# Kernel optimization log

Measured on AMD Instinct MI355X. Metric: run time of the kernel, lower is better.

The kernel has to match this reference:

```python
import jax, jax.numpy as jnp
import numpy as np

H_IMG, W_IMG = 32, 32   # img_dim
HID = 256               # hidden_size
B = 128                 # batch


def setup_inputs() -> dict:
    key = jax.random.key(0)
    k1, k2, k3, k4 = jax.random.split(key, 4)
    x = jax.random.normal(k1, (B, H_IMG * W_IMG), dtype=jnp.float32)
    w_ih = jax.random.normal(k2, (4 * HID, 1), dtype=jnp.float32) * 0.1
    w_hh = jax.random.normal(k3, (4 * HID, HID), dtype=jnp.float32) * 0.05
    bias = jax.random.normal(k4, (4 * HID,), dtype=jnp.float32) * 0.1
    return {"x": x, "w_ih": w_ih, "w_hh": w_hh, "bias": bias}


def _mdlstm(x, w_ih, w_hh, bias):
    # x: [B, H*W] in row-major pixel order (pixel_idx = row*W + col)
    Bb = x.shape[0]
    xg = x.reshape(Bb, H_IMG, W_IMG).transpose(1, 2, 0)  # [H, W, B]
    wih_vec = w_ih[:, 0]  # input_size == 1 -> linear is scalar * row-vector

    def cell(x_pix, h_up, s_up, h_left, s_left):
        # Same weight_hh is applied to both directional hidden states; for
        # boundary pixels the corresponding h/s are zeros, so the gating in
        # the original code (skip when row==0 / col==0) holds identically.
        gates = (x_pix[:, None] * wih_vec[None, :]
                 + (h_up + h_left) @ w_hh.T
                 + bias)                                  # [B, 4*HID]
        i, f, g, o = jnp.split(gates, 4, axis=1)
        i = jax.nn.sigmoid(i)
        f = jax.nn.sigmoid(f)
        g = jnp.tanh(g)
        o = jax.nn.sigmoid(o)
        s = f * (s_up + s_left) + i * g                   # shared forgetgate for both dims
        h = o * jnp.tanh(s)
        return h, s

    zeros = jnp.zeros((Bb, HID), x.dtype)

    def row_step(carry, x_row):
        h_up_row, s_up_row = carry                        # [W, B, HID] each

        def col_step(c, inp):
            h_left, s_left = c
            x_pix, h_up, s_up = inp
            h, s = cell(x_pix, h_up, s_up, h_left, s_left)
            return (h, s), (h, s)

        _, (h_row, s_row) = jax.lax.scan(col_step, (zeros, zeros),
                                         (x_row, h_up_row, s_up_row))
        return (h_row, s_row), h_row

    init = (jnp.zeros((W_IMG, Bb, HID), x.dtype),
            jnp.zeros((W_IMG, Bb, HID), x.dtype))
    _, h_all = jax.lax.scan(row_step, init, xg)           # [H, W, B, HID]
    # torch.cat(h_matrix, 1): pixels ordered row-major, each [B, HID]
    return h_all.transpose(2, 0, 1, 3).reshape(Bb, H_IMG * W_IMG * HID)


def reference(x, w_ih, w_hh, bias):
    return _mdlstm(x, w_ih, w_hh, bias)
```

## Files before the change

### kernel.cpp

```cpp
#include <hip/hip_runtime.h>
#include <math.h>


#define HIMG 32
#define WIMG 32
#define BATCH 128
#define HID 256
#define BH (BATCH * HID)
#define SLAB (32 * 128 * 256)

#define WSTRIDE 136

typedef double f64x4 __attribute__((ext_vector_type(4)));

__global__ __launch_bounds__(256, 4)
void mdlstm_diag_kernel(const float* __restrict__ x,
                        const float* __restrict__ wih,
                        const float* __restrict__ whh,
                        const float* __restrict__ bias,
                        float* __restrict__ out,
                        double* __restrict__ hbuf,
                        double* __restrict__ sbuf,
                        int d, int rlo)
{
    __shared__ double lds[4096];
    double* A_lds = lds;
    float*  W_lds = (float*)(lds + 1024);
    double* G_lds = lds;

    const int tid = threadIdx.x;
    const int id  = blockIdx.x;
    const int cellIdx = id >> 5;
    const int tileIdx = id & 31;
    const int ktile = tileIdx & 7;
    const int b4    = tileIdx >> 3;
    const int k0 = ktile * 32;
    const int b0 = b4 * 32;

    const int r = rlo + cellIdx;
    const int c = d - r;
    const int rc = r * WIMG + c;

    const int prev = (d & 1) ^ 1;
    const int cur  = d & 1;
    const double* hp = hbuf + (size_t)prev * SLAB;
    const double* sp = sbuf + (size_t)prev * SLAB;
    double* hc = hbuf + (size_t)cur * SLAB;
    double* sc = sbuf + (size_t)cur * SLAB;

    const bool has_up   = (r > 0);
    const bool has_left = (c > 0);
    const double* hu = hp + (size_t)(r - 1) * BH;
    const double* hl = hp + (size_t)r * BH;

    const int lane = tid & 63;
    const int wid  = tid >> 6;
    const int wb0  = (wid & 1) * 16;
    const int wf0  = (wid >> 1) * 64;
    const int cc   = lane & 15;
    const int gg   = lane >> 4;

    int layout;
    {
        double pa = (cc == 1) ? 1.0 : 0.0;
        double pb = (cc == 2) ? 1.0 : 0.0;
        f64x4 pc = {0.0, 0.0, 0.0, 0.0};
        pc = __builtin_amdgcn_mfma_f64_16x16x4f64(pa, pb, pc, 0, 0, 0);
        double s = fabs(pc[0]) + fabs(pc[1]) + fabs(pc[2]) + fabs(pc[3]);
        #pragma unroll
        for (int off = 32; off > 0; off >>= 1) s += __shfl_xor(s, off, 64);
        unsigned long long h0 = __ballot(lane == 2  && pc[1] == 4.0);
        unsigned long long h1 = __ballot(lane == 18 && pc[0] == 4.0);
        unsigned long long h2 = __ballot(lane == 1  && pc[2] == 4.0);
        unsigned long long h3 = __ballot(lane == 33 && pc[0] == 4.0);
        layout = -1;
        if (s == 4.0) {
            if (h0) layout = 0;
            else if (h1) layout = 1;
            else if (h2) layout = 2;
            else if (h3) layout = 3;
        }
    }
    const bool use_mfma = (layout >= 0);

    const int a_row = tid >> 4;
    const int a_kp  = tid & 15;
    const size_t ga0 = (size_t)(b0 + a_row) * HID + 2 * a_kp;
    const size_t ga1 = ga0 + (size_t)16 * HID;
    const float* w_src[4];
    int w_phi[4], w_kq[4];
    #pragma unroll
    for (int p = 0; p < 4; p++) {
        int u = tid + p * 256;
        int phi = u >> 3, kq = u & 7;
        int F = (phi >> 5) * 256 + k0 + (phi & 31);
        w_src[p] = whh + (size_t)F * HID + 4 * kq;
        w_phi[p] = phi; w_kq[p] = kq;
    }

    f64x4 acc[4];
    #pragma unroll
    for (int ft = 0; ft < 4; ft++) acc[ft] = (f64x4){0.0, 0.0, 0.0, 0.0};

    double2 pu0, pu1, pl0, pl1;
    float4 pw[4];
    {
        const double2 z = {0.0, 0.0};
        pu0 = has_up   ? *(const double2*)(hu + ga0) : z;
        pu1 = has_up   ? *(const double2*)(hu + ga1) : z;
        pl0 = has_left ? *(const double2*)(hl + ga0) : z;
        pl1 = has_left ? *(const double2*)(hl + ga1) : z;
        #pragma unroll
        for (int p = 0; p < 4; p++)
            pw[p] = *(const float4*)(w_src[p]);
    }

    for (int ck = 0; ck < 8; ck++) {
        __syncthreads();
        {
            const int k = 2 * a_kp;
            const double s0x = pu0.x + pl0.x, s0y = pu0.y + pl0.y;
            const double s1x = pu1.x + pl1.x, s1y = pu1.y + pl1.y;
            A_lds[ k      * 32 + ((a_row      + k    ) & 31)] = s0x;
            A_lds[(k + 1) * 32 + ((a_row      + k + 1) & 31)] = s0y;
            A_lds[ k      * 32 + ((a_row + 16 + k    ) & 31)] = s1x;
            A_lds[(k + 1) * 32 + ((a_row + 16 + k + 1) & 31)] = s1y;
        }
        #pragma unroll
        for (int p = 0; p < 4; p++) {
            const int kb = 4 * w_kq[p];
            W_lds[(kb + 0) * WSTRIDE + w_phi[p]] = pw[p].x;
            W_lds[(kb + 1) * WSTRIDE + w_phi[p]] = pw[p].y;
            W_lds[(kb + 2) * WSTRIDE + w_phi[p]] = pw[p].z;
            W_lds[(kb + 3) * WSTRIDE + w_phi[p]] = pw[p].w;
        }
        __syncthreads();

        if (ck < 7) {
            const int kg = (ck + 1) * 32;
            const double2 z = {0.0, 0.0};
            pu0 = has_up   ? *(const double2*)(hu + ga0 + kg) : z;
            pu1 = has_up   ? *(const double2*)(hu + ga1 + kg) : z;
            pl0 = has_left ? *(const double2*)(hl + ga0 + kg) : z;
            pl1 = has_left ? *(const double2*)(hl + ga1 + kg) : z;
            #pragma unroll
            for (int p = 0; p < 4; p++)
                pw[p] = *(const float4*)(w_src[p] + kg);
        }

        if (use_mfma) {
            #pragma unroll
            for (int t = 0; t < 8; t++) {
                const int kq = t * 4 + gg;
                const double aval = A_lds[kq * 32 + ((wb0 + cc + kq) & 31)];
                const float* wrow = &W_lds[kq * WSTRIDE + wf0 + cc];
                #pragma unroll
                for (int ft = 0; ft < 4; ft++) {
                    const double bval = (double)wrow[ft * 16];
                    acc[ft] = __builtin_amdgcn_mfma_f64_16x16x4f64(aval, bval, acc[ft], 0, 0, 0);
                }
            }
        } else {
            for (int k = 0; k < 32; k++) {
                double av[4], wv4[4];
                #pragma unroll
                for (int b = 0; b < 4; b++)
                    av[b] = A_lds[k * 32 + ((wb0 + 4 * gg + b + k) & 31)];
                #pragma unroll
                for (int ft = 0; ft < 4; ft++)
                    wv4[ft] = (double)W_lds[k * WSTRIDE + wf0 + ft * 16 + cc];
                #pragma unroll
                for (int ft = 0; ft < 4; ft++)
                    #pragma unroll
                    for (int b = 0; b < 4; b++)
                        acc[ft][b] = fma(av[b], wv4[ft], acc[ft][b]);
            }
        }
    }

    __syncthreads();
    const int slay = use_mfma ? layout : 0;
    #pragma unroll
    for (int ft = 0; ft < 4; ft++) {
        #pragma unroll
        for (int b = 0; b < 4; b++) {
            const int rA = (slay & 1) ? (gg + 4 * b) : (4 * gg + b);
            const int m  = (slay >= 2) ? cc : rA;
            const int n  = (slay >= 2) ? rA : cc;
            const int phi  = wf0 + ft * 16 + n;
            const int brow = wb0 + m;
            G_lds[phi * 32 + ((brow + phi) & 31)] = acc[ft][b];
        }
    }
    __syncthreads();

    const int ec = tid & 31;
    const int eb = tid >> 5;
    const int k = k0 + ec;
    double wv[4], bv[4];
    #pragma unroll
    for (int g = 0; g < 4; g++) {
        wv[g] = (double)wih[g * 256 + k];
        bv[g] = (double)bias[g * 256 + k];
    }
    #pragma unroll
    for (int i = 0; i < 4; i++) {
        const int bl = eb + 8 * i;
        const int b = b0 + bl;
        double gate[4];
        #pragma unroll
        for (int g = 0; g < 4; g++) {
            const int phi = g * 32 + ec;
            gate[g] = G_lds[phi * 32 + ((bl + phi) & 31)];
        }
        const double xp = (double)x[b * (HIMG * WIMG) + rc];
        const double su = has_up   ? sp[(size_t)(r - 1) * BH + b * HID + k] : 0.0;
        const double sl = has_left ? sp[(size_t)r * BH + b * HID + k]       : 0.0;
        const double gi = gate[0] + xp * wv[0] + bv[0];
        const double gf = gate[1] + xp * wv[1] + bv[1];
        const double gg2 = gate[2] + xp * wv[2] + bv[2];
        const double go = gate[3] + xp * wv[3] + bv[3];
        const double iv = 1.0 / (1.0 + exp(-gi));
        const double fv = 1.0 / (1.0 + exp(-gf));
        const double gv = tanh(gg2);
        const double ov = 1.0 / (1.0 + exp(-go));
        const double sv = fv * (su + sl) + iv * gv;
        const double hv = ov * tanh(sv);
        sc[(size_t)r * BH + b * HID + k] = sv;
        hc[(size_t)r * BH + b * HID + k] = hv;
        out[(size_t)b * (HIMG * WIMG * HID) + (size_t)rc * HID + k] = (float)hv;
    }
}

extern "C" void kernel_launch(void* const* d_in, const int* in_sizes, int n_in,
                              void* d_out, int out_size, void* d_ws, size_t ws_size,
                              hipStream_t stream) {
    const float* x    = (const float*)d_in[0];
    const float* wih  = (const float*)d_in[1];
    const float* whh  = (const float*)d_in[2];
    const float* bias = (const float*)d_in[3];
    float* out = (float*)d_out;

    double* hbuf = (double*)d_ws;
    double* sbuf = hbuf + (size_t)2 * SLAB;

    for (int d = 0; d < HIMG + WIMG - 1; d++) {
        int rlo = d - (WIMG - 1); if (rlo < 0) rlo = 0;
        int rhi = d < (HIMG - 1) ? d : (HIMG - 1);
        int nc = rhi - rlo + 1;
        mdlstm_diag_kernel<<<dim3(nc * 32), 256, 0, stream>>>(
            x, wih, whh, bias, out, hbuf, sbuf, d, rlo);
    }
}
```

Baseline: 3.143 ms.

## Replace per-diagonal kernel launches with a persistent cooperative kernel using grid sync

Replaces the 63 separate per-anti-diagonal kernel launches with a single persistent cooperative kernel of 1024 blocks. It loops over diagonals internally and uses grid.sync between them. Per-block setup (MFMA layout probe, input-weight and bias loads) is hoisted out of the diagonal loop. This removes launch overhead and repeated setup, but every block must wait at each grid barrier even when idle on short diagonals. If cooperative launch is unavailable or occupancy is insufficient, it falls back to the old multi-launch path.

```diff
diff --git a/kernel.cpp b/kernel.cpp
--- a/kernel.cpp
+++ b/kernel.cpp
@@ -1,4 +1,5 @@
 #include <hip/hip_runtime.h>
+#include <hip/hip_cooperative_groups.h>
 #include <math.h>
 
 
@@ -13,15 +14,16 @@
 
 typedef double f64x4 __attribute__((ext_vector_type(4)));
 
+namespace cg = cooperative_groups;
+
 __global__ __launch_bounds__(256, 4)
-void mdlstm_diag_kernel(const float* __restrict__ x,
-                        const float* __restrict__ wih,
-                        const float* __restrict__ whh,
-                        const float* __restrict__ bias,
-                        float* __restrict__ out,
-                        double* __restrict__ hbuf,
-                        double* __restrict__ sbuf,
-                        int d, int rlo)
+void mdlstm_persistent(const float* __restrict__ x,
+                       const float* __restrict__ wih,
+                       const float* __restrict__ whh,
+                       const float* __restrict__ bias,
+                       float* __restrict__ out,
+                       double* __restrict__ hbuf,
+                       double* __restrict__ sbuf)
 {
     __shared__ double lds[4096];
     double* A_lds = lds;
@@ -29,29 +31,13 @@
     double* G_lds = lds;
 
     const int tid = threadIdx.x;
-    const int id  = blockIdx.x;
-    const int cellIdx = id >> 5;
-    const int tileIdx = id & 31;
+    const int bid = blockIdx.x;
+    const int cellSlot = bid >> 5;
+    const int tileIdx = bid & 31;
     const int ktile = tileIdx & 7;
     const int b4    = tileIdx >> 3;
     const int k0 = ktile * 32;
     const int b0 = b4 * 32;
-
-    const int r = rlo + cellIdx;
-    const int c = d - r;
-    const int rc = r * WIMG + c;
-
-    const int prev = (d & 1) ^ 1;
-    const int cur  = d & 1;
-    const double* hp = hbuf + (size_t)prev * SLAB;
-    const double* sp = sbuf + (size_t)prev * SLAB;
-    double* hc = hbuf + (size_t)cur * SLAB;
-    double* sc = sbuf + (size_t)cur * SLAB;
-
-    const bool has_up   = (r > 0);
-    const bool has_left = (c > 0);
-    const double* hu = hp + (size_t)(r - 1) * BH;
-    const double* hl = hp + (size_t)r * BH;
 
     const int lane = tid & 63;
     const int wid  = tid >> 6;
@@ -82,6 +68,261 @@
         }
     }
     const bool use_mfma = (layout >= 0);
+    const int slay = use_mfma ? layout : 0;
+
+    const int a_row = tid >> 4;
+    const int a_kp  = tid & 15;
+    const size_t ga0 = (size_t)(b0 + a_row) * HID + 2 * a_kp;
+    const size_t ga1 = ga0 + (size_t)16 * HID;
+    const float* w_src[4];
+    int w_phi[4], w_kq[4];
+    #pragma unroll
+    for (int p = 0; p < 4; p++) {
+        int u = tid + p * 256;
+        int phi = u >> 3, kq = u & 7;
+        int F = (phi >> 5) * 256 + k0 + (phi & 31);
+        w_src[p] = whh + (size_t)F * HID + 4 * kq;
+        w_phi[p] = phi; w_kq[p] = kq;
+    }
+
+    const int ec = tid & 31;
+    const int eb = tid >> 5;
+    const int kE = k0 + ec;
+    double wvE[4], bvE[4];
+    #pragma unroll
+    for (int g = 0; g < 4; g++) {
+        wvE[g] = (double)wih[g * 256 + kE];
+        bvE[g] = (double)bias[g * 256 + kE];
+    }
+
+    cg::grid_group grid = cg::this_grid();
+
+    for (int d = 0; d < HIMG + WIMG - 1; d++) {
+        int rlo = d - (WIMG - 1); if (rlo < 0) rlo = 0;
+        int rhi = d < (HIMG - 1) ? d : (HIMG - 1);
+        int nc = rhi - rlo + 1;
+
+        if (cellSlot < nc) {
+            const int r = rlo + cellSlot;
+            const int c = d - r;
+            const int rc = r * WIMG + c;
+
+            const int prev = (d & 1) ^ 1;
+            const int cur  = d & 1;
+            const double* hp = hbuf + (size_t)prev * SLAB;
+            const double* sp = sbuf + (size_t)prev * SLAB;
+            double* hc = hbuf + (size_t)cur * SLAB;
+            double* sc = sbuf + (size_t)cur * SLAB;
+
+            const bool has_up   = (r > 0);
+            const bool has_left = (c > 0);
+            const double* hu = hp + (size_t)(r - 1) * BH;
+            const double* hl = hp + (size_t)r * BH;
+
+            f64x4 acc[4];
+            #pragma unroll
+            for (int ft = 0; ft < 4; ft++) acc[ft] = (f64x4){0.0, 0.0, 0.0, 0.0};
+
+            double2 pu0, pu1, pl0, pl1;
+            float4 pw[4];
+            {
+                const double2 z = {0.0, 0.0};
+                pu0 = has_up   ? *(const double2*)(hu + ga0) : z;
+                pu1 = has_up   ? *(const double2*)(hu + ga1) : z;
+                pl0 = has_left ? *(const double2*)(hl + ga0) : z;
+                pl1 = has_left ? *(const double2*)(hl + ga1) : z;
+                #pragma unroll
+                for (int p = 0; p < 4; p++)
+                    pw[p] = *(const float4*)(w_src[p]);
+            }
+
+            for (int ck = 0; ck < 8; ck++) {
+                __syncthreads();
+                {
+                    const int k = 2 * a_kp;
+                    const double s0x = pu0.x + pl0.x, s0y = pu0.y + pl0.y;
+                    const double s1x = pu1.x + pl1.x, s1y = pu1.y + pl1.y;
+                    A_lds[ k      * 32 + ((a_row      + k    ) & 31)] = s0x;
+                    A_lds[(k + 1) * 32 + ((a_row      + k + 1) & 31)] = s0y;
+                    A_lds[ k      * 32 + ((a_row + 16 + k    ) & 31)] = s1x;
+                    A_lds[(k + 1) * 32 + ((a_row + 16 + k + 1) & 31)] = s1y;
+                }
+                #pragma unroll
+                for (int p = 0; p < 4; p++) {
+                    const int kb = 4 * w_kq[p];
+                    W_lds[(kb + 0) * WSTRIDE + w_phi[p]] = pw[p].x;
+                    W_lds[(kb + 1) * WSTRIDE + w_phi[p]] = pw[p].y;
+                    W_lds[(kb + 2) * WSTRIDE + w_phi[p]] = pw[p].z;
+                    W_lds[(kb + 3) * WSTRIDE + w_phi[p]] = pw[p].w;
+                }
+                __syncthreads();
+
+                if (ck < 7) {
+                    const int kg = (ck + 1) * 32;
+                    const double2 z = {0.0, 0.0};
+                    pu0 = has_up   ? *(const double2*)(hu + ga0 + kg) : z;
+                    pu1 = has_up   ? *(const double2*)(hu + ga1 + kg) : z;
+                    pl0 = has_left ? *(const double2*)(hl + ga0 + kg) : z;
+                    pl1 = has_left ? *(const double2*)(hl + ga1 + kg) : z;
+                    #pragma unroll
+                    for (int p = 0; p < 4; p++)
+                        pw[p] = *(const float4*)(w_src[p] + kg);
+                }
+
+                if (use_mfma) {
+                    #pragma unroll
+                    for (int t = 0; t < 8; t++) {
+                        const int kq = t * 4 + gg;
+                        const double aval = A_lds[kq * 32 + ((wb0 + cc + kq) & 31)];
+                        const float* wrow = &W_lds[kq * WSTRIDE + wf0 + cc];
+                        #pragma unroll
+                        for (int ft = 0; ft < 4; ft++) {
+                            const double bval = (double)wrow[ft * 16];
+                            acc[ft] = __builtin_amdgcn_mfma_f64_16x16x4f64(aval, bval, acc[ft], 0, 0, 0);
+                        }
+                    }
+                } else {
+                    for (int k = 0; k < 32; k++) {
+                        double av[4], wv4[4];
+                        #pragma unroll
+                        for (int b = 0; b < 4; b++)
+                            av[b] = A_lds[k * 32 + ((wb0 + 4 * gg + b + k) & 31)];
+                        #pragma unroll
+                        for (int ft = 0; ft < 4; ft++)
+                            wv4[ft] = (double)W_lds[k * WSTRIDE + wf0 + ft * 16 + cc];
+                        #pragma unroll
+                        for (int ft = 0; ft < 4; ft++)
+                            #pragma unroll
+                            for (int b = 0; b < 4; b++)
+                                acc[ft][b] = fma(av[b], wv4[ft], acc[ft][b]);
+                    }
+                }
+            }
+
+            double xp4[4], su4[4], sl4[4];
+            #pragma unroll
+            for (int i = 0; i < 4; i++) {
+                const int b = b0 + eb + 8 * i;
+                xp4[i] = (double)x[b * (HIMG * WIMG) + rc];
+                su4[i] = has_up   ? sp[(size_t)(r - 1) * BH + b * HID + kE] : 0.0;
+                sl4[i] = has_left ? sp[(size_t)r * BH + b * HID + kE]       : 0.0;
+            }
+
+            __syncthreads();
+            #pragma unroll
+            for (int ft = 0; ft < 4; ft++) {
+                #pragma unroll
+                for (int b = 0; b < 4; b++) {
+                    const int rA = (slay & 1) ? (gg + 4 * b) : (4 * gg + b);
+                    const int m  = (slay >= 2) ? cc : rA;
+                    const int n  = (slay >= 2) ? rA : cc;
+                    const int phi  = wf0 + ft * 16 + n;
+                    const int brow = wb0 + m;
+                    G_lds[phi * 32 + ((brow + phi) & 31)] = acc[ft][b];
+                }
+            }
+            __syncthreads();
+
+            #pragma unroll
+            for (int i = 0; i < 4; i++) {
+                const int bl = eb + 8 * i;
+                const int b = b0 + bl;
+                double gate[4];
+                #pragma unroll
+                for (int g = 0; g < 4; g++) {
+                    const int phi = g * 32 + ec;
+                    gate[g] = G_lds[phi * 32 + ((bl + phi) & 31)];
+                }
+                const double gi = gate[0] + xp4[i] * wvE[0] + bvE[0];
+                const double gf = gate[1] + xp4[i] * wvE[1] + bvE[1];
+                const double gG = gate[2] + xp4[i] * wvE[2] + bvE[2];
+                const double go = gate[3] + xp4[i] * wvE[3] + bvE[3];
+                const double iv = 1.0 / (1.0 + exp(-gi));
+                const double fv = 1.0 / (1.0 + exp(-gf));
+                const double gv = tanh(gG);
+                const double ov = 1.0 / (1.0 + exp(-go));
+                const double sv = fv * (su4[i] + sl4[i]) + iv * gv;
+                const double hv = ov * tanh(sv);
+                sc[(size_t)r * BH + b * HID + kE] = sv;
+                hc[(size_t)r * BH + b * HID + kE] = hv;
+                out[(size_t)b * (HIMG * WIMG * HID) + (size_t)rc * HID + kE] = (float)hv;
+            }
+        }
+
+        __threadfence();
+        grid.sync();
+    }
+}
+
+__global__ __launch_bounds__(256, 4)
+void mdlstm_diag_kernel(const float* __restrict__ x,
+                        const float* __restrict__ wih,
+                        const float* __restrict__ whh,
+                        const float* __restrict__ bias,
+                        float* __restrict__ out,
+                        double* __restrict__ hbuf,
+                        double* __restrict__ sbuf,
+                        int d, int rlo)
+{
+    __shared__ double lds[4096];
+    double* A_lds = lds;
+    float*  W_lds = (float*)(lds + 1024);
+    double* G_lds = lds;
+
+    const int tid = threadIdx.x;
+    const int id  = blockIdx.x;
+    const int cellIdx = id >> 5;
+    const int tileIdx = id & 31;
+    const int ktile = tileIdx & 7;
+    const int b4    = tileIdx >> 3;
+    const int k0 = ktile * 32;
+    const int b0 = b4 * 32;
+
+    const int r = rlo + cellIdx;
+    const int c = d - r;
+    const int rc = r * WIMG + c;
+
+    const int prev = (d & 1) ^ 1;
+    const int cur  = d & 1;
+    const double* hp = hbuf + (size_t)prev * SLAB;
+    const double* sp = sbuf + (size_t)prev * SLAB;
+    double* hc = hbuf + (size_t)cur * SLAB;
+    double* sc = sbuf + (size_t)cur * SLAB;
+
+    const bool has_up   = (r > 0);
+    const bool has_left = (c > 0);
+    const double* hu = hp + (size_t)(r - 1) * BH;
+    const double* hl = hp + (size_t)r * BH;
+
+    const int lane = tid & 63;
+    const int wid  = tid >> 6;
+    const int wb0  = (wid & 1) * 16;
+    const int wf0  = (wid >> 1) * 64;
+    const int cc   = lane & 15;
+    const int gg   = lane >> 4;
+
+    int layout;
+    {
+        double pa = (cc == 1) ? 1.0 : 0.0;
+        double pb = (cc == 2) ? 1.0 : 0.0;
+        f64x4 pc = {0.0, 0.0, 0.0, 0.0};
+        pc = __builtin_amdgcn_mfma_f64_16x16x4f64(pa, pb, pc, 0, 0, 0);
+        double s = fabs(pc[0]) + fabs(pc[1]) + fabs(pc[2]) + fabs(pc[3]);
+        #pragma unroll
+        for (int off = 32; off > 0; off >>= 1) s += __shfl_xor(s, off, 64);
+        unsigned long long h0 = __ballot(lane == 2  && pc[1] == 4.0);
+        unsigned long long h1 = __ballot(lane == 18 && pc[0] == 4.0);
+        unsigned long long h2 = __ballot(lane == 1  && pc[2] == 4.0);
+        unsigned long long h3 = __ballot(lane == 33 && pc[0] == 4.0);
+        layout = -1;
+        if (s == 4.0) {
+            if (h0) layout = 0;
+            else if (h1) layout = 1;
+            else if (h2) layout = 2;
+            else if (h3) layout = 3;
+        }
+    }
+    const bool use_mfma = (layout >= 0);
 
     const int a_row = tid >> 4;
     const int a_kp  = tid & 15;
@@ -244,6 +485,23 @@
     double* hbuf = (double*)d_ws;
     double* sbuf = hbuf + (size_t)2 * SLAB;
 
+    static int coop = -1;
+    if (coop < 0) {
+        int maxB = 0;
+        hipError_t e = hipOccupancyMaxActiveBlocksPerMultiprocessor(
+            &maxB, mdlstm_persistent, 256, 0);
+        coop = (e == hipSuccess && maxB >= 4) ? 1 : 0;
+    }
+
+    if (coop) {
+        void* args[] = {(void*)&x, (void*)&wih, (void*)&whh, (void*)&bias,
+                        (void*)&out, (void*)&hbuf, (void*)&sbuf};
+        hipError_t e = hipLaunchCooperativeKernel(
+            mdlstm_persistent, dim3(1024), dim3(256), args, 0, stream);
+        if (e == hipSuccess) return;
+        coop = 0;
+    }
+
     for (int d = 0; d < HIMG + WIMG - 1; d++) {
         int rlo = d - (WIMG - 1); if (rlo < 0) rlo = 0;
         int rhi = d < (HIMG - 1) ? d : (HIMG - 1);
```

Measured after the change: 3.112 ms. No clear change (-1.0%).

## Remap block indices for XCD locality, vectorize W LDS stores, prefetch epilogue loads

Applied to the files above, without the earlier changes.

Block indices are remapped so that the eight consecutive blocks (id & 7) land on different (cell, batch-tile) groups sharing the same k-tile, which aims to improve L2 reuse of the w_hh slices across the XCDs. The grid is padded to a multiple of 64, and surplus blocks return early. The W tile in LDS is transposed to a phi-major layout with stride 36, so each thread stores it with one float4 write instead of four scalar writes. The x and previous cell-state loads for the epilogue are issued before the G_lds write barrier so their latency overlaps the MFMA drain, at the cost of extra registers.

```diff
diff --git a/kernel.cpp b/kernel.cpp
--- a/kernel.cpp
+++ b/kernel.cpp
@@ -9,7 +9,7 @@
 #define BH (BATCH * HID)
 #define SLAB (32 * 128 * 256)
 
-#define WSTRIDE 136
+#define PSTR 36
 
 typedef double f64x4 __attribute__((ext_vector_type(4)));
 
@@ -21,7 +21,7 @@
                         float* __restrict__ out,
                         double* __restrict__ hbuf,
                         double* __restrict__ sbuf,
-                        int d, int rlo)
+                        int d, int rlo, int nc)
 {
     __shared__ double lds[4096];
     double* A_lds = lds;
@@ -30,10 +30,15 @@
 
     const int tid = threadIdx.x;
     const int id  = blockIdx.x;
-    const int cellIdx = id >> 5;
-    const int tileIdx = id & 31;
-    const int ktile = tileIdx & 7;
-    const int b4    = tileIdx >> 3;
+
+    const int rx    = id & 7;
+    const int q     = id >> 3;
+    const int ktile = q & 7;
+    const int ghi   = q >> 3;
+    const int g     = ghi * 8 + rx;
+    if (g >= nc * 4) return;
+    const int cellIdx = g >> 2;
+    const int b4      = g & 3;
     const int k0 = ktile * 32;
     const int b0 = b4 * 32;
 
@@ -88,14 +93,14 @@
     const size_t ga0 = (size_t)(b0 + a_row) * HID + 2 * a_kp;
     const size_t ga1 = ga0 + (size_t)16 * HID;
     const float* w_src[4];
-    int w_phi[4], w_kq[4];
+    int w_pos[4];
     #pragma unroll
     for (int p = 0; p < 4; p++) {
         int u = tid + p * 256;
         int phi = u >> 3, kq = u & 7;
         int F = (phi >> 5) * 256 + k0 + (phi & 31);
         w_src[p] = whh + (size_t)F * HID + 4 * kq;
-        w_phi[p] = phi; w_kq[p] = kq;
+        w_pos[p] = phi * PSTR + 4 * kq;
     }
 
     f64x4 acc[4];
@@ -114,6 +119,8 @@
         for (int p = 0; p < 4; p++)
             pw[p] = *(const float4*)(w_src[p]);
     }
+
+    const float* wbase = &W_lds[(wf0 + cc) * PSTR + gg];
 
     for (int ck = 0; ck < 8; ck++) {
         __syncthreads();
@@ -127,13 +134,8 @@
             A_lds[(k + 1) * 32 + ((a_row + 16 + k + 1) & 31)] = s1y;
         }
         #pragma unroll
-        for (int p = 0; p < 4; p++) {
-            const int kb = 4 * w_kq[p];
-            W_lds[(kb + 0) * WSTRIDE + w_phi[p]] = pw[p].x;
-            W_lds[(kb + 1) * WSTRIDE + w_phi[p]] = pw[p].y;
-            W_lds[(kb + 2) * WSTRIDE + w_phi[p]] = pw[p].z;
-            W_lds[(kb + 3) * WSTRIDE + w_phi[p]] = pw[p].w;
-        }
+        for (int p = 0; p < 4; p++)
+            *(float4*)&W_lds[w_pos[p]] = pw[p];
         __syncthreads();
 
         if (ck < 7) {
@@ -153,10 +155,9 @@
             for (int t = 0; t < 8; t++) {
                 const int kq = t * 4 + gg;
                 const double aval = A_lds[kq * 32 + ((wb0 + cc + kq) & 31)];
-                const float* wrow = &W_lds[kq * WSTRIDE + wf0 + cc];
                 #pragma unroll
                 for (int ft = 0; ft < 4; ft++) {
-                    const double bval = (double)wrow[ft * 16];
+                    const double bval = (double)wbase[ft * (16 * PSTR) + 4 * t];
                     acc[ft] = __builtin_amdgcn_mfma_f64_16x16x4f64(aval, bval, acc[ft], 0, 0, 0);
                 }
             }
@@ -168,7 +169,7 @@
                     av[b] = A_lds[k * 32 + ((wb0 + 4 * gg + b + k) & 31)];
                 #pragma unroll
                 for (int ft = 0; ft < 4; ft++)
-                    wv4[ft] = (double)W_lds[k * WSTRIDE + wf0 + ft * 16 + cc];
+                    wv4[ft] = (double)W_lds[(wf0 + ft * 16 + cc) * PSTR + k];
                 #pragma unroll
                 for (int ft = 0; ft < 4; ft++)
                     #pragma unroll
@@ -176,6 +177,18 @@
                         acc[ft][b] = fma(av[b], wv4[ft], acc[ft][b]);
             }
         }
+    }
+
+    const int ec = tid & 31;
+    const int eb = tid >> 5;
+    const int kE = k0 + ec;
+    double xp4[4], su4[4], sl4[4];
+    #pragma unroll
+    for (int i = 0; i < 4; i++) {
+        const int b = b0 + eb + 8 * i;
+        xp4[i] = (double)x[b * (HIMG * WIMG) + rc];
+        su4[i] = has_up   ? sp[(size_t)(r - 1) * BH + b * HID + kE] : 0.0;
+        sl4[i] = has_left ? sp[(size_t)r * BH + b * HID + kE]       : 0.0;
     }
 
     __syncthreads();
@@ -194,14 +207,11 @@
     }
     __syncthreads();
 
-    const int ec = tid & 31;
-    const int eb = tid >> 5;
-    const int k = k0 + ec;
     double wv[4], bv[4];
     #pragma unroll
-    for (int g = 0; g < 4; g++) {
-        wv[g] = (double)wih[g * 256 + k];
-        bv[g] = (double)bias[g * 256 + k];
+    for (int g2 = 0; g2 < 4; g2++) {
+        wv[g2] = (double)wih[g2 * 256 + kE];
+        bv[g2] = (double)bias[g2 * 256 + kE];
     }
     #pragma unroll
     for (int i = 0; i < 4; i++) {
@@ -209,26 +219,23 @@
         const int b = b0 + bl;
         double gate[4];
         #pragma unroll
-        for (int g = 0; g < 4; g++) {
-            const int phi = g * 32 + ec;
-            gate[g] = G_lds[phi * 32 + ((bl + phi) & 31)];
-        }
-        const double xp = (double)x[b * (HIMG * WIMG) + rc];
-        const double su = has_up   ? sp[(size_t)(r - 1) * BH + b * HID + k] : 0.0;
-        const double sl = has_left ? sp[(size_t)r * BH + b * HID + k]       : 0.0;
-        const double gi = gate[0] + xp * wv[0] + bv[0];
-        const double gf = gate[1] + xp * wv[1] + bv[1];
-        const double gg2 = gate[2] + xp * wv[2] + bv[2];
-        const double go = gate[3] + xp * wv[3] + bv[3];
+        for (int g2 = 0; g2 < 4; g2++) {
+            const int phi = g2 * 32 + ec;
+            gate[g2] = G_lds[phi * 32 + ((bl + phi) & 31)];
+        }
+        const double gi = gate[0] + xp4[i] * wv[0] + bv[0];
+        const double gf = gate[1] + xp4[i] * wv[1] + bv[1];
+        const double gG = gate[2] + xp4[i] * wv[2] + bv[2];
+        const double go = gate[3] + xp4[i] * wv[3] + bv[3];
         const double iv = 1.0 / (1.0 + exp(-gi));
         const double fv = 1.0 / (1.0 + exp(-gf));
-        const double gv = tanh(gg2);
+        const double gv = tanh(gG);
         const double ov = 1.0 / (1.0 + exp(-go));
-        const double sv = fv * (su + sl) + iv * gv;
+        const double sv = fv * (su4[i] + sl4[i]) + iv * gv;
         const double hv = ov * tanh(sv);
-        sc[(size_t)r * BH + b * HID + k] = sv;
-        hc[(size_t)r * BH + b * HID + k] = hv;
-        out[(size_t)b * (HIMG * WIMG * HID) + (size_t)rc * HID + k] = (float)hv;
+        sc[(size_t)r * BH + b * HID + kE] = sv;
+        hc[(size_t)r * BH + b * HID + kE] = hv;
+        out[(size_t)b * (HIMG * WIMG * HID) + (size_t)rc * HID + kE] = (float)hv;
     }
 }
 
@@ -248,7 +255,8 @@
         int rlo = d - (WIMG - 1); if (rlo < 0) rlo = 0;
         int rhi = d < (HIMG - 1) ? d : (HIMG - 1);
         int nc = rhi - rlo + 1;
-        mdlstm_diag_kernel<<<dim3(nc * 32), 256, 0, stream>>>(
-            x, wih, whh, bias, out, hbuf, sbuf, d, rlo);
+        int g8 = (4 * nc + 7) / 8;
+        mdlstm_diag_kernel<<<dim3(g8 * 64), 256, 0, stream>>>(
+            x, wih, whh, bias, out, hbuf, sbuf, d, rlo, nc);
     }
 }
```

Result: no change. 3.167 ms (+0.8%).
